# Kernel tuning notes

Measured on AMD Instinct MI355X. Metric: run time of the kernel, lower is better.

## Reference

```python
import jax, jax.numpy as jnp
import numpy as np

B = 1048576
NUM_USERS = 200000
NUM_ITEMS = 100000
NUM_GROUPS = 50000
D = 32  # embedding_dim; grp_forward hardcodes 4*32 reshape -> 3 members per group


def setup_inputs() -> dict:
    key = jax.random.key(0)
    ks = jax.random.split(key, 12)
    return {
        "group_inputs": jax.random.randint(ks[0], (B,), 0, NUM_GROUPS, dtype=jnp.int32),
        "item_inputs": jax.random.randint(ks[1], (B,), 0, NUM_ITEMS, dtype=jnp.int32),
        "group_members": jax.random.randint(ks[2], (NUM_GROUPS, 3), 0, NUM_USERS, dtype=jnp.int32),
        "user_emb": jax.random.normal(ks[3], (NUM_USERS, D), dtype=jnp.float32) * 0.1,
        "item_emb": jax.random.normal(ks[4], (NUM_ITEMS, D), dtype=jnp.float32) * 0.1,
        "att_w1": jax.random.normal(ks[5], (4 * D, 16), dtype=jnp.float32) * 0.1,
        "att_b1": jnp.zeros((16,), dtype=jnp.float32),
        "att_w2": jax.random.normal(ks[6], (16, 3), dtype=jnp.float32) * 0.1,
        "att_b2": jnp.zeros((3,), dtype=jnp.float32),
        "pred_w1": jax.random.normal(ks[7], (3 * D, 8), dtype=jnp.float32) * 0.1,
        "pred_b1": jnp.zeros((8,), dtype=jnp.float32),
        "pred_w2": jax.random.normal(ks[8], (8, 1), dtype=jnp.float32) * 0.1,
        "pred_b2": jnp.zeros((1,), dtype=jnp.float32),
    }


def reference(group_inputs, item_inputs, group_members,
              user_emb, item_emb,
              att_w1, att_b1, att_w2, att_b2,
              pred_w1, pred_b1, pred_w2, pred_b2):
    # Vectorized form of AGREE.grp_forward (3 members per group, dropout=0 eval)
    members = group_members[group_inputs]            # [B, 3]
    me = user_emb[members]                            # [B, 3, D] member embeds
    ie = item_emb[item_inputs]                        # [B, D]
    # concat(members, item) along member dim, flatten to [B, 4D]
    x = jnp.concatenate([me.reshape(-1, 3 * D), ie], axis=1)  # [B, 4D]
    h = jax.nn.relu(x @ att_w1 + att_b1)              # [B, 16]
    wt = jax.nn.softmax(h @ att_w2 + att_b2, axis=1)  # [B, 3] attention weights
    g = jnp.einsum('bm,bmd->bd', wt, me)              # [B, D] attended group embed
    new = jnp.concatenate([g * ie, g, ie], axis=1)    # [B, 3D]
    h2 = jax.nn.relu(new @ pred_w1 + pred_b1)         # [B, 8]
    y = jax.nn.sigmoid(h2 @ pred_w2 + pred_b2)        # [B, 1]
    return y
```

## Files before the change

kernel.cpp:

```cpp
#include <hip/hip_runtime.h>
#include <math.h>


#define DD 32

__global__ __launch_bounds__(256) void agree_fwd(
    const int* __restrict__ gi, const int* __restrict__ ii,
    const int* __restrict__ gm,
    const float* __restrict__ ue, const float* __restrict__ itemb,
    const float* __restrict__ w1, const float* __restrict__ b1,
    const float* __restrict__ w2, const float* __restrict__ b2,
    const float* __restrict__ pw1, const float* __restrict__ pb1,
    const float* __restrict__ pw2, const float* __restrict__ pb2,
    float* __restrict__ out, int B)
{
    int b = blockIdx.x * blockDim.x + threadIdx.x;
    if (b >= B) return;

    int g  = gi[b];
    int it = ii[b];
    int m0 = gm[3 * g + 0];
    int m1 = gm[3 * g + 1];
    int m2 = gm[3 * g + 2];

    float me[3][DD];
    float iev[DD];
    {
        const float4* p0 = reinterpret_cast<const float4*>(ue + (size_t)m0 * DD);
        const float4* p1 = reinterpret_cast<const float4*>(ue + (size_t)m1 * DD);
        const float4* p2 = reinterpret_cast<const float4*>(ue + (size_t)m2 * DD);
        const float4* p3 = reinterpret_cast<const float4*>(itemb + (size_t)it * DD);
        #pragma unroll
        for (int q = 0; q < DD / 4; ++q) {
            float4 v0 = p0[q];
            float4 v1 = p1[q];
            float4 v2 = p2[q];
            float4 v3 = p3[q];
            me[0][4*q+0] = v0.x; me[0][4*q+1] = v0.y; me[0][4*q+2] = v0.z; me[0][4*q+3] = v0.w;
            me[1][4*q+0] = v1.x; me[1][4*q+1] = v1.y; me[1][4*q+2] = v1.z; me[1][4*q+3] = v1.w;
            me[2][4*q+0] = v2.x; me[2][4*q+1] = v2.y; me[2][4*q+2] = v2.z; me[2][4*q+3] = v2.w;
            iev[4*q+0]   = v3.x; iev[4*q+1]   = v3.y; iev[4*q+2]   = v3.z; iev[4*q+3]   = v3.w;
        }
    }

    float h[16];
    #pragma unroll
    for (int j = 0; j < 16; ++j) h[j] = b1[j];

    #pragma unroll
    for (int m = 0; m < 3; ++m) {
        #pragma unroll
        for (int k = 0; k < DD; ++k) {
            float xk = me[m][k];
            #pragma unroll
            for (int j = 0; j < 16; ++j)
                h[j] = fmaf(xk, w1[(m * DD + k) * 16 + j], h[j]);
        }
    }
    #pragma unroll
    for (int k = 0; k < DD; ++k) {
        float xk = iev[k];
        #pragma unroll
        for (int j = 0; j < 16; ++j)
            h[j] = fmaf(xk, w1[(3 * DD + k) * 16 + j], h[j]);
    }
    #pragma unroll
    for (int j = 0; j < 16; ++j) h[j] = fmaxf(h[j], 0.0f);

    float l0 = b2[0], l1 = b2[1], l2 = b2[2];
    #pragma unroll
    for (int j = 0; j < 16; ++j) {
        l0 = fmaf(h[j], w2[j * 3 + 0], l0);
        l1 = fmaf(h[j], w2[j * 3 + 1], l1);
        l2 = fmaf(h[j], w2[j * 3 + 2], l2);
    }
    float mx = fmaxf(l0, fmaxf(l1, l2));
    float e0 = __expf(l0 - mx);
    float e1 = __expf(l1 - mx);
    float e2 = __expf(l2 - mx);
    float inv = 1.0f / (e0 + e1 + e2);
    float wt0 = e0 * inv, wt1 = e1 * inv, wt2 = e2 * inv;

    float h2[8];
    #pragma unroll
    for (int j = 0; j < 8; ++j) h2[j] = pb1[j];

    #pragma unroll
    for (int d = 0; d < DD; ++d) {
        float gd  = wt0 * me[0][d] + wt1 * me[1][d] + wt2 * me[2][d];
        float gie = gd * iev[d];
        #pragma unroll
        for (int j = 0; j < 8; ++j) {
            h2[j] = fmaf(gie,    pw1[d * 8 + j],            h2[j]);
            h2[j] = fmaf(gd,     pw1[(DD + d) * 8 + j],     h2[j]);
            h2[j] = fmaf(iev[d], pw1[(2 * DD + d) * 8 + j], h2[j]);
        }
    }

    float z = pb2[0];
    #pragma unroll
    for (int j = 0; j < 8; ++j)
        z = fmaf(fmaxf(h2[j], 0.0f), pw2[j], z);

    out[b] = 1.0f / (1.0f + __expf(-z));
}

extern "C" void kernel_launch(void* const* d_in, const int* in_sizes, int n_in,
                              void* d_out, int out_size, void* d_ws, size_t ws_size,
                              hipStream_t stream) {
    int B = in_sizes[0];
    dim3 block(256);
    dim3 grid((B + 255) / 256);
    hipLaunchKernelGGL(agree_fwd, grid, block, 0, stream,
        (const int*)d_in[0],
        (const int*)d_in[1],
        (const int*)d_in[2],
        (const float*)d_in[3],
        (const float*)d_in[4],
        (const float*)d_in[5],
        (const float*)d_in[6],
        (const float*)d_in[7],
        (const float*)d_in[8],
        (const float*)d_in[9],
        (const float*)d_in[10],
        (const float*)d_in[11],
        (const float*)d_in[12],
        (float*)d_out, B);
}
```

Baseline: 221.3 us.

## Precompute per-group and per-item linear projections before the batch kernel

Adds two precompute kernels that build, for each group, the attention pre-activation partial sum, each member's projection through the second predictor block, and the member embeddings; and, for each item, its attention partial sum, its predictor projection plus bias, and its embedding. The main kernel then gathers one group record and one item record per sample, which removes most of the per-sample matmul FLOPs and the double indirection through group_members. In exchange it writes and reads a workspace of roughly 34 MB and adds two launches. The old fused kernel is kept as a fallback when the workspace is too small.

```diff
diff --git a/kernel.cpp b/kernel.cpp
--- a/kernel.cpp
+++ b/kernel.cpp
@@ -1,8 +1,188 @@
 #include <hip/hip_runtime.h>
 #include <math.h>
 
-
 #define DD 32
+#define GREC 136
+#define IREC 56
+
+__global__ __launch_bounds__(256) void grp_pre(
+    const int* __restrict__ gm, const float* __restrict__ ue,
+    const float* __restrict__ w1, const float* __restrict__ b1,
+    const float* __restrict__ pw1,
+    float* __restrict__ grec, int NG)
+{
+    int g = blockIdx.x * blockDim.x + threadIdx.x;
+    if (g >= NG) return;
+    float* rec = grec + (size_t)g * GREC;
+
+    float s[16];
+    #pragma unroll
+    for (int j = 0; j < 16; ++j) s[j] = b1[j];
+
+    #pragma unroll
+    for (int m = 0; m < 3; ++m) {
+        int u = gm[3 * g + m];
+        const float4* p = reinterpret_cast<const float4*>(ue + (size_t)u * DD);
+        float mv[DD];
+        #pragma unroll
+        for (int q = 0; q < 8; ++q) {
+            float4 v = p[q];
+            mv[4*q] = v.x; mv[4*q+1] = v.y; mv[4*q+2] = v.z; mv[4*q+3] = v.w;
+        }
+        float Pm[8];
+        #pragma unroll
+        for (int j = 0; j < 8; ++j) Pm[j] = 0.0f;
+        #pragma unroll
+        for (int d = 0; d < DD; ++d) {
+            float x = mv[d];
+            #pragma unroll
+            for (int j = 0; j < 16; ++j)
+                s[j] = fmaf(x, w1[(m * DD + d) * 16 + j], s[j]);
+            #pragma unroll
+            for (int j = 0; j < 8; ++j)
+                Pm[j] = fmaf(x, pw1[(DD + d) * 8 + j], Pm[j]);
+        }
+        reinterpret_cast<float4*>(rec + 16 + m * 8)[0] = make_float4(Pm[0], Pm[1], Pm[2], Pm[3]);
+        reinterpret_cast<float4*>(rec + 16 + m * 8)[1] = make_float4(Pm[4], Pm[5], Pm[6], Pm[7]);
+        #pragma unroll
+        for (int q = 0; q < 8; ++q)
+            reinterpret_cast<float4*>(rec + 40 + m * DD)[q] =
+                make_float4(mv[4*q], mv[4*q+1], mv[4*q+2], mv[4*q+3]);
+    }
+    #pragma unroll
+    for (int q = 0; q < 4; ++q)
+        reinterpret_cast<float4*>(rec)[q] = make_float4(s[4*q], s[4*q+1], s[4*q+2], s[4*q+3]);
+}
+
+__global__ __launch_bounds__(256) void item_pre(
+    const float* __restrict__ itemb,
+    const float* __restrict__ w1,
+    const float* __restrict__ pw1, const float* __restrict__ pb1,
+    float* __restrict__ irec, int NI)
+{
+    int i = blockIdx.x * blockDim.x + threadIdx.x;
+    if (i >= NI) return;
+    float* rec = irec + (size_t)i * IREC;
+
+    const float4* p = reinterpret_cast<const float4*>(itemb + (size_t)i * DD);
+    float ev[DD];
+    #pragma unroll
+    for (int q = 0; q < 8; ++q) {
+        float4 v = p[q];
+        ev[4*q] = v.x; ev[4*q+1] = v.y; ev[4*q+2] = v.z; ev[4*q+3] = v.w;
+    }
+    float t[16];
+    #pragma unroll
+    for (int j = 0; j < 16; ++j) t[j] = 0.0f;
+    float Q[8];
+    #pragma unroll
+    for (int j = 0; j < 8; ++j) Q[j] = pb1[j];
+    #pragma unroll
+    for (int d = 0; d < DD; ++d) {
+        float x = ev[d];
+        #pragma unroll
+        for (int j = 0; j < 16; ++j)
+            t[j] = fmaf(x, w1[(3 * DD + d) * 16 + j], t[j]);
+        #pragma unroll
+        for (int j = 0; j < 8; ++j)
+            Q[j] = fmaf(x, pw1[(2 * DD + d) * 8 + j], Q[j]);
+    }
+    #pragma unroll
+    for (int q = 0; q < 4; ++q)
+        reinterpret_cast<float4*>(rec)[q] = make_float4(t[4*q], t[4*q+1], t[4*q+2], t[4*q+3]);
+    reinterpret_cast<float4*>(rec + 16)[0] = make_float4(Q[0], Q[1], Q[2], Q[3]);
+    reinterpret_cast<float4*>(rec + 16)[1] = make_float4(Q[4], Q[5], Q[6], Q[7]);
+    #pragma unroll
+    for (int q = 0; q < 8; ++q)
+        reinterpret_cast<float4*>(rec + 24)[q] = make_float4(ev[4*q], ev[4*q+1], ev[4*q+2], ev[4*q+3]);
+}
+
+__global__ __launch_bounds__(256) void agree_main(
+    const int* __restrict__ gi, const int* __restrict__ ii,
+    const float* __restrict__ grec, const float* __restrict__ irec,
+    const float* __restrict__ w2, const float* __restrict__ b2,
+    const float* __restrict__ pw1, const float* __restrict__ pw2,
+    const float* __restrict__ pb2,
+    float* __restrict__ out, int B)
+{
+    int b = blockIdx.x * blockDim.x + threadIdx.x;
+    if (b >= B) return;
+
+    const float* gr = grec + (size_t)gi[b] * GREC;
+    const float* ir = irec + (size_t)ii[b] * IREC;
+    const float4* gr4 = reinterpret_cast<const float4*>(gr);
+    const float4* ir4 = reinterpret_cast<const float4*>(ir);
+
+    float h[16];
+    #pragma unroll
+    for (int q = 0; q < 4; ++q) {
+        float4 a = gr4[q];
+        float4 c = ir4[q];
+        h[4*q+0] = fmaxf(a.x + c.x, 0.0f);
+        h[4*q+1] = fmaxf(a.y + c.y, 0.0f);
+        h[4*q+2] = fmaxf(a.z + c.z, 0.0f);
+        h[4*q+3] = fmaxf(a.w + c.w, 0.0f);
+    }
+
+    float l0 = b2[0], l1 = b2[1], l2 = b2[2];
+    #pragma unroll
+    for (int j = 0; j < 16; ++j) {
+        l0 = fmaf(h[j], w2[j * 3 + 0], l0);
+        l1 = fmaf(h[j], w2[j * 3 + 1], l1);
+        l2 = fmaf(h[j], w2[j * 3 + 2], l2);
+    }
+    float mx = fmaxf(l0, fmaxf(l1, l2));
+    float e0 = __expf(l0 - mx);
+    float e1 = __expf(l1 - mx);
+    float e2 = __expf(l2 - mx);
+    float inv = 1.0f / (e0 + e1 + e2);
+    float wt0 = e0 * inv, wt1 = e1 * inv, wt2 = e2 * inv;
+
+    float h2[8];
+    {
+        float4 q0 = ir4[4], q1 = ir4[5];
+        h2[0] = q0.x; h2[1] = q0.y; h2[2] = q0.z; h2[3] = q0.w;
+        h2[4] = q1.x; h2[5] = q1.y; h2[6] = q1.z; h2[7] = q1.w;
+    }
+    #pragma unroll
+    for (int m = 0; m < 3; ++m) {
+        float wm = (m == 0) ? wt0 : (m == 1) ? wt1 : wt2;
+        float4 p0 = gr4[4 + 2 * m];
+        float4 p1 = gr4[5 + 2 * m];
+        h2[0] = fmaf(wm, p0.x, h2[0]); h2[1] = fmaf(wm, p0.y, h2[1]);
+        h2[2] = fmaf(wm, p0.z, h2[2]); h2[3] = fmaf(wm, p0.w, h2[3]);
+        h2[4] = fmaf(wm, p1.x, h2[4]); h2[5] = fmaf(wm, p1.y, h2[5]);
+        h2[6] = fmaf(wm, p1.z, h2[6]); h2[7] = fmaf(wm, p1.w, h2[7]);
+    }
+
+    const float4* me4 = reinterpret_cast<const float4*>(gr + 40);
+    const float4* ie4 = reinterpret_cast<const float4*>(ir + 24);
+    #pragma unroll
+    for (int q = 0; q < 8; ++q) {
+        float4 a0 = me4[q];
+        float4 a1 = me4[8 + q];
+        float4 a2 = me4[16 + q];
+        float4 e  = ie4[q];
+        float g0 = fmaf(wt0, a0.x, fmaf(wt1, a1.x, wt2 * a2.x)) * e.x;
+        float g1 = fmaf(wt0, a0.y, fmaf(wt1, a1.y, wt2 * a2.y)) * e.y;
+        float g2 = fmaf(wt0, a0.z, fmaf(wt1, a1.z, wt2 * a2.z)) * e.z;
+        float g3 = fmaf(wt0, a0.w, fmaf(wt1, a1.w, wt2 * a2.w)) * e.w;
+        #pragma unroll
+        for (int j = 0; j < 8; ++j) {
+            h2[j] = fmaf(g0, pw1[(4*q+0) * 8 + j], h2[j]);
+            h2[j] = fmaf(g1, pw1[(4*q+1) * 8 + j], h2[j]);
+            h2[j] = fmaf(g2, pw1[(4*q+2) * 8 + j], h2[j]);
+            h2[j] = fmaf(g3, pw1[(4*q+3) * 8 + j], h2[j]);
+        }
+    }
+
+    float z = pb2[0];
+    #pragma unroll
+    for (int j = 0; j < 8; ++j)
+        z = fmaf(fmaxf(h2[j], 0.0f), pw2[j], z);
+
+    out[b] = 1.0f / (1.0f + __expf(-z));
+}
 
 __global__ __launch_bounds__(256) void agree_fwd(
     const int* __restrict__ gi, const int* __restrict__ ii,
@@ -16,114 +196,111 @@
 {
     int b = blockIdx.x * blockDim.x + threadIdx.x;
     if (b >= B) return;
-
-    int g  = gi[b];
-    int it = ii[b];
-    int m0 = gm[3 * g + 0];
-    int m1 = gm[3 * g + 1];
-    int m2 = gm[3 * g + 2];
-
-    float me[3][DD];
-    float iev[DD];
+    int g = gi[b], it = ii[b];
+    int m0 = gm[3*g+0], m1 = gm[3*g+1], m2 = gm[3*g+2];
+    float me[3][DD], iev[DD];
     {
         const float4* p0 = reinterpret_cast<const float4*>(ue + (size_t)m0 * DD);
         const float4* p1 = reinterpret_cast<const float4*>(ue + (size_t)m1 * DD);
         const float4* p2 = reinterpret_cast<const float4*>(ue + (size_t)m2 * DD);
         const float4* p3 = reinterpret_cast<const float4*>(itemb + (size_t)it * DD);
         #pragma unroll
-        for (int q = 0; q < DD / 4; ++q) {
-            float4 v0 = p0[q];
-            float4 v1 = p1[q];
-            float4 v2 = p2[q];
-            float4 v3 = p3[q];
-            me[0][4*q+0] = v0.x; me[0][4*q+1] = v0.y; me[0][4*q+2] = v0.z; me[0][4*q+3] = v0.w;
-            me[1][4*q+0] = v1.x; me[1][4*q+1] = v1.y; me[1][4*q+2] = v1.z; me[1][4*q+3] = v1.w;
-            me[2][4*q+0] = v2.x; me[2][4*q+1] = v2.y; me[2][4*q+2] = v2.z; me[2][4*q+3] = v2.w;
-            iev[4*q+0]   = v3.x; iev[4*q+1]   = v3.y; iev[4*q+2]   = v3.z; iev[4*q+3]   = v3.w;
-        }
-    }
-
+        for (int q = 0; q < 8; ++q) {
+            float4 v0 = p0[q], v1 = p1[q], v2 = p2[q], v3 = p3[q];
+            me[0][4*q]=v0.x; me[0][4*q+1]=v0.y; me[0][4*q+2]=v0.z; me[0][4*q+3]=v0.w;
+            me[1][4*q]=v1.x; me[1][4*q+1]=v1.y; me[1][4*q+2]=v1.z; me[1][4*q+3]=v1.w;
+            me[2][4*q]=v2.x; me[2][4*q+1]=v2.y; me[2][4*q+2]=v2.z; me[2][4*q+3]=v2.w;
+            iev[4*q]=v3.x; iev[4*q+1]=v3.y; iev[4*q+2]=v3.z; iev[4*q+3]=v3.w;
+        }
+    }
     float h[16];
     #pragma unroll
     for (int j = 0; j < 16; ++j) h[j] = b1[j];
-
-    #pragma unroll
-    for (int m = 0; m < 3; ++m) {
+    #pragma unroll
+    for (int m = 0; m < 3; ++m)
         #pragma unroll
         for (int k = 0; k < DD; ++k) {
             float xk = me[m][k];
             #pragma unroll
             for (int j = 0; j < 16; ++j)
-                h[j] = fmaf(xk, w1[(m * DD + k) * 16 + j], h[j]);
-        }
-    }
+                h[j] = fmaf(xk, w1[(m*DD+k)*16+j], h[j]);
+        }
     #pragma unroll
     for (int k = 0; k < DD; ++k) {
         float xk = iev[k];
         #pragma unroll
         for (int j = 0; j < 16; ++j)
-            h[j] = fmaf(xk, w1[(3 * DD + k) * 16 + j], h[j]);
+            h[j] = fmaf(xk, w1[(3*DD+k)*16+j], h[j]);
     }
     #pragma unroll
     for (int j = 0; j < 16; ++j) h[j] = fmaxf(h[j], 0.0f);
-
     float l0 = b2[0], l1 = b2[1], l2 = b2[2];
     #pragma unroll
     for (int j = 0; j < 16; ++j) {
-        l0 = fmaf(h[j], w2[j * 3 + 0], l0);
-        l1 = fmaf(h[j], w2[j * 3 + 1], l1);
-        l2 = fmaf(h[j], w2[j * 3 + 2], l2);
+        l0 = fmaf(h[j], w2[j*3+0], l0);
+        l1 = fmaf(h[j], w2[j*3+1], l1);
+        l2 = fmaf(h[j], w2[j*3+2], l2);
     }
     float mx = fmaxf(l0, fmaxf(l1, l2));
-    float e0 = __expf(l0 - mx);
-    float e1 = __expf(l1 - mx);
-    float e2 = __expf(l2 - mx);
-    float inv = 1.0f / (e0 + e1 + e2);
-    float wt0 = e0 * inv, wt1 = e1 * inv, wt2 = e2 * inv;
-
+    float e0 = __expf(l0-mx), e1 = __expf(l1-mx), e2 = __expf(l2-mx);
+    float inv = 1.0f / (e0+e1+e2);
+    float wt0 = e0*inv, wt1 = e1*inv, wt2 = e2*inv;
     float h2[8];
     #pragma unroll
     for (int j = 0; j < 8; ++j) h2[j] = pb1[j];
-
     #pragma unroll
     for (int d = 0; d < DD; ++d) {
-        float gd  = wt0 * me[0][d] + wt1 * me[1][d] + wt2 * me[2][d];
+        float gd  = wt0*me[0][d] + wt1*me[1][d] + wt2*me[2][d];
         float gie = gd * iev[d];
         #pragma unroll
         for (int j = 0; j < 8; ++j) {
-            h2[j] = fmaf(gie,    pw1[d * 8 + j],            h2[j]);
-            h2[j] = fmaf(gd,     pw1[(DD + d) * 8 + j],     h2[j]);
-            h2[j] = fmaf(iev[d], pw1[(2 * DD + d) * 8 + j], h2[j]);
-        }
-    }
-
+            h2[j] = fmaf(gie,    pw1[d*8+j],          h2[j]);
+            h2[j] = fmaf(gd,     pw1[(DD+d)*8+j],     h2[j]);
+            h2[j] = fmaf(iev[d], pw1[(2*DD+d)*8+j],   h2[j]);
+        }
+    }
     float z = pb2[0];
     #pragma unroll
     for (int j = 0; j < 8; ++j)
         z = fmaf(fmaxf(h2[j], 0.0f), pw2[j], z);
-
     out[b] = 1.0f / (1.0f + __expf(-z));
 }
 
 extern "C" void kernel_launch(void* const* d_in, const int* in_sizes, int n_in,
                               void* d_out, int out_size, void* d_ws, size_t ws_size,
                               hipStream_t stream) {
-    int B = in_sizes[0];
-    dim3 block(256);
-    dim3 grid((B + 255) / 256);
-    hipLaunchKernelGGL(agree_fwd, grid, block, 0, stream,
-        (const int*)d_in[0],
-        (const int*)d_in[1],
-        (const int*)d_in[2],
-        (const float*)d_in[3],
-        (const float*)d_in[4],
-        (const float*)d_in[5],
-        (const float*)d_in[6],
-        (const float*)d_in[7],
-        (const float*)d_in[8],
-        (const float*)d_in[9],
-        (const float*)d_in[10],
-        (const float*)d_in[11],
-        (const float*)d_in[12],
-        (float*)d_out, B);
-}
+    const int*   gi    = (const int*)d_in[0];
+    const int*   ii    = (const int*)d_in[1];
+    const int*   gm    = (const int*)d_in[2];
+    const float* ue    = (const float*)d_in[3];
+    const float* itemb = (const float*)d_in[4];
+    const float* w1    = (const float*)d_in[5];
+    const float* b1    = (const float*)d_in[6];
+    const float* w2    = (const float*)d_in[7];
+    const float* b2    = (const float*)d_in[8];
+    const float* pw1   = (const float*)d_in[9];
+    const float* pb1   = (const float*)d_in[10];
+    const float* pw2   = (const float*)d_in[11];
+    const float* pb2   = (const float*)d_in[12];
+    float* out = (float*)d_out;
+
+    int B  = in_sizes[0];
+    int NG = in_sizes[2] / 3;
+    int NI = in_sizes[4] / DD;
+
+    size_t need = ((size_t)NG * GREC + (size_t)NI * IREC) * sizeof(float);
+    if (ws_size >= need) {
+        float* grec = (float*)d_ws;
+        float* irec = grec + (size_t)NG * GREC;
+        hipLaunchKernelGGL(grp_pre, dim3((NG + 255) / 256), dim3(256), 0, stream,
+                           gm, ue, w1, b1, pw1, grec, NG);
+        hipLaunchKernelGGL(item_pre, dim3((NI + 255) / 256), dim3(256), 0, stream,
+                           itemb, w1, pw1, pb1, irec, NI);
+        hipLaunchKernelGGL(agree_main, dim3((B + 255) / 256), dim3(256), 0, stream,
+                           gi, ii, grec, irec, w2, b2, pw1, pw2, pb2, out, B);
+    } else {
+        hipLaunchKernelGGL(agree_fwd, dim3((B + 255) / 256), dim3(256), 0, stream,
+                           gi, ii, gm, ue, itemb, w1, b1, w2, b2,
+                           pw1, pb1, pw2, pb2, out, B);
+    }
+}
```

Measured after the change: 407.4 us. 84.1% more time.
